# Kernel optimization log

Measured on AMD Instinct MI355X. Metric: run time of the kernel, lower is better.

The kernel has to match this reference:

```python
import jax, jax.numpy as jnp
import numpy as np

N_NODES = 50000
N_EDGES = 1600000
NUM_BASIS = 10
HIDDEN = 64
MAX_RADIUS = 3.0
WEIGHT_NUMEL = 5  # paths: (0x0->0),(0x1->1),(1x0->1),(1x1->0),(1x1->1)


def setup_inputs() -> dict:
    key = jax.random.key(0)
    k1, k2, k3, k4, k5 = jax.random.split(key, 5)
    f_1 = jax.random.normal(k1, (N_NODES, 4), dtype=jnp.float32)
    pos = jax.random.uniform(k2, (N_NODES, 3), dtype=jnp.float32) * MAX_RADIUS
    edge_index = jax.random.randint(k3, (2, N_EDGES), 0, N_NODES, dtype=jnp.int64)
    # radial MLP params (e3nn FullyConnectedNet init: std-normal weights)
    W1 = jax.random.normal(k4, (NUM_BASIS, HIDDEN), dtype=jnp.float32)
    W2 = jax.random.normal(k5, (HIDDEN, WEIGHT_NUMEL), dtype=jnp.float32)
    return {"f_1": f_1, "pos": pos, "W1": W1, "W2": W2, "edge_index": edge_index}


def _forward(f_1, pos, W1, W2, edge_index):
    row, col = edge_index[0], edge_index[1]
    num_nodes = f_1.shape[0]
    num_neighbors = edge_index.shape[1] / num_nodes

    edge_vec = pos[row] - pos[col]                      # [E,3]
    r2 = jnp.sum(edge_vec * edge_vec, axis=-1)
    r = jnp.sqrt(jnp.maximum(r2, 1e-12))                # [E]
    unit = edge_vec / r[:, None]

    # spherical harmonics 0e+1e, component normalization, e3nn (y,z,x) order
    sh = jnp.concatenate(
        [jnp.ones_like(unit[:, :1]), jnp.sqrt(3.0) * unit[:, [1, 2, 0]]], axis=-1
    )                                                   # [E,4]

    # soft_one_hot_linspace, basis='smooth_finite', cutoff=True
    values = jnp.linspace(0.0, MAX_RADIUS, NUM_BASIS + 2)[1:-1]
    step = values[1] - values[0]
    diff = (r[:, None] - values) / step                 # [E,num_basis]
    inside = jnp.abs(diff) < 1.0
    d = jnp.where(inside, diff, 0.0)
    C = 1.14136 * float(np.e) ** 2
    emb = jnp.where(inside, C * jnp.exp(-1.0 / (1.0 + d) - 1.0 / (1.0 - d)), 0.0)

    # e3nn FullyConnectedNet [num_basis, hidden, weight_numel] with relu
    # hidden: act normalized to unit 2nd moment (relu -> *sqrt(2)); weights /sqrt(fan_in)
    h = jax.nn.relu(emb @ (W1 / jnp.sqrt(float(NUM_BASIS)))) * jnp.sqrt(2.0)
    w = h @ (W2 / jnp.sqrt(float(HIDDEN)))              # [E,5]

    # FullyConnectedTensorProduct (0e+1e) x (0e+1e) -> (0e+1e), per-edge weights
    x = f_1[row]
    x0, xv = x[:, 0], x[:, 1:4]
    y0, yv = sh[:, 0], sh[:, 1:4]
    inv_s3 = 1.0 / jnp.sqrt(3.0)
    inv_s6 = 1.0 / jnp.sqrt(6.0)
    # output 0e: fan-in 2 paths -> norm sqrt(1/2)
    out0 = jnp.sqrt(0.5) * (
        w[:, 0] * x0 * y0 + w[:, 3] * jnp.sum(xv * yv, axis=-1) * inv_s3
    )
    # output 1e: fan-in 3 paths -> norm sqrt(3/3)=1
    outv = (
        w[:, 1:2] * x0[:, None] * yv * inv_s3
        + w[:, 2:3] * xv * y0[:, None] * inv_s3
        + w[:, 4:5] * jnp.cross(xv, yv) * inv_s6
    )
    f_edge = jnp.concatenate([out0[:, None], outv], axis=-1)  # [E,4]

    out = jax.ops.segment_sum(f_edge, col, num_segments=num_nodes)
    return out / jnp.sqrt(num_neighbors).astype(out.dtype)


def reference(f_1, pos, W1, W2, edge_index):
    return _forward(f_1, pos, W1, W2, edge_index)
```

## Files before the change

### kernel.cpp

```cpp
#include <hip/hip_runtime.h>
#include <math.h>

#define N_NODES_C 50000
#define N_EDGES_C 1600000
#define EPB3 4096
#define NBLK_E3 391
#define NBLK_N 196
#define TBL 256

#define NREG 49
#define NREGP 64
#define RSH 10
#define RNODES 1024
#define CAPL 16
#define NCHG 16

#define QSCALE 1024.0f
#define QINV   (1.0f / 1024.0f)

__device__ __forceinline__ int detect_is64_block(const void* eidx, int t, int* lds_flag) {
    if (t < 64) {
        const long long* p = (const long long*)eidx;
        bool ok = true;
        for (int k = 0; k < 4; ++k) {
            long long v = p[t * 4 + k];
            ok &= (v >= 0 && v < (long long)N_NODES_C);
        }
        unsigned long long m = __ballot(ok);
        if (t == 0) *lds_flag = (m == ~0ull) ? 1 : 0;
    }
    __syncthreads();
    return *lds_flag;
}

__device__ __forceinline__ int load_col(const void* eidx, int is64, int e) {
    return is64 ? (int)((const long long*)eidx)[N_EDGES_C + e]
                : ((const int*)eidx)[N_EDGES_C + e];
}
__device__ __forceinline__ int load_row(const void* eidx, int is64, int e) {
    return is64 ? (int)((const long long*)eidx)[e]
                : ((const int*)eidx)[e];
}

__device__ __forceinline__ void edge_quant(const float* __restrict__ f1,
                                           const float* __restrict__ pos,
                                           const float* __restrict__ w1s,
                                           const float* __restrict__ W2,
                                           int row, int col, int v[4]) {
    v[0] = v[1] = v[2] = v[3] = 0;
    float px = pos[row * 3 + 0] - pos[col * 3 + 0];
    float py = pos[row * 3 + 1] - pos[col * 3 + 1];
    float pz = pos[row * 3 + 2] - pos[col * 3 + 2];
    float r2 = px * px + py * py + pz * pz;
    float r = sqrtf(fmaxf(r2, 1e-12f));
    float inv_r = 1.0f / r;
    float ux = px * inv_r, uy = py * inv_r, uz = pz * inv_r;
    const float SQ3 = 1.7320508075688772f;
    float yv0 = SQ3 * uy, yv1 = SQ3 * uz, yv2 = SQ3 * ux;

    const float C = 8.433573069075486f;
    float tt = r * (11.0f / 3.0f);
    int k1 = (int)tt;
    float d = tt - (float)k1;
    float e0 = 0.f, e1 = 0.f;
    int b0 = 0, b1 = 0;
    if (k1 >= 1 && k1 <= 10) {
        b0 = k1 - 1;
        e0 = C * __expf(-1.0f / (1.0f + d) - 1.0f / (1.0f - d));
    }
    int k2 = k1 + 1;
    if (k2 <= 10 && d > 0.f) {
        b1 = k2 - 1;
        float d2 = d - 1.0f;
        e1 = C * __expf(-1.0f / (1.0f + d2) - 1.0f / (1.0f - d2));
    }
    if (e0 == 0.f && e1 == 0.f) return;

    const float* r0 = &w1s[b0 * 68];
    const float* r1 = &w1s[b1 * 68];
    float w0 = 0.f, w1a = 0.f, w2a = 0.f, w3 = 0.f, w4 = 0.f;
#pragma unroll
    for (int j = 0; j < 64; j += 4) {
        float4 a = *(const float4*)(r0 + j);
        float4 b = *(const float4*)(r1 + j);
        float h0 = fmaxf(e0 * a.x + e1 * b.x, 0.f);
        float h1 = fmaxf(e0 * a.y + e1 * b.y, 0.f);
        float h2 = fmaxf(e0 * a.z + e1 * b.z, 0.f);
        float h3 = fmaxf(e0 * a.w + e1 * b.w, 0.f);
        w0  += h0 * W2[(j + 0) * 5 + 0] + h1 * W2[(j + 1) * 5 + 0] + h2 * W2[(j + 2) * 5 + 0] + h3 * W2[(j + 3) * 5 + 0];
        w1a += h0 * W2[(j + 0) * 5 + 1] + h1 * W2[(j + 1) * 5 + 1] + h2 * W2[(j + 2) * 5 + 1] + h3 * W2[(j + 3) * 5 + 1];
        w2a += h0 * W2[(j + 0) * 5 + 2] + h1 * W2[(j + 1) * 5 + 2] + h2 * W2[(j + 2) * 5 + 2] + h3 * W2[(j + 3) * 5 + 2];
        w3  += h0 * W2[(j + 0) * 5 + 3] + h1 * W2[(j + 1) * 5 + 3] + h2 * W2[(j + 2) * 5 + 3] + h3 * W2[(j + 3) * 5 + 3];
        w4  += h0 * W2[(j + 0) * 5 + 4] + h1 * W2[(j + 1) * 5 + 4] + h2 * W2[(j + 2) * 5 + 4] + h3 * W2[(j + 3) * 5 + 4];
    }
    const float SC = 0.05590169943749474f;
    w0 *= SC; w1a *= SC; w2a *= SC; w3 *= SC; w4 *= SC;

    float4 x = *(const float4*)(f1 + row * 4);
    float x0 = x.x, xv0 = x.y, xv1 = x.z, xv2 = x.w;

    const float INV_S3 = 0.5773502691896258f;
    const float INV_S6 = 0.4082482904638631f;
    const float SQH    = 0.7071067811865476f;
    const float INV_SQRT_NN = 0.17677669529663687f;

    float dotxy = xv0 * yv0 + xv1 * yv1 + xv2 * yv2;
    float out0 = SQH * (w0 * x0 + w3 * dotxy * INV_S3) * INV_SQRT_NN;
    float cx0 = xv1 * yv2 - xv2 * yv1;
    float cx1 = xv2 * yv0 - xv0 * yv2;
    float cx2 = xv0 * yv1 - xv1 * yv0;
    float o1 = (w1a * x0 * yv0 * INV_S3 + w2a * xv0 * INV_S3 + w4 * cx0 * INV_S6) * INV_SQRT_NN;
    float o2 = (w1a * x0 * yv1 * INV_S3 + w2a * xv1 * INV_S3 + w4 * cx1 * INV_S6) * INV_SQRT_NN;
    float o3 = (w1a * x0 * yv2 * INV_S3 + w2a * xv2 * INV_S3 + w4 * cx2 * INV_S6) * INV_SQRT_NN;

    v[0] = min(8191, max(-8191, (int)rintf(out0 * QSCALE)));
    v[1] = min(8191, max(-8191, (int)rintf(o1   * QSCALE)));
    v[2] = min(8191, max(-8191, (int)rintf(o2   * QSCALE)));
    v[3] = min(8191, max(-8191, (int)rintf(o3   * QSCALE)));
}

__device__ __forceinline__ unsigned long long edge_q(
        float prx, float pry, float prz, float4 xx,
        float pcx, float pcy, float pcz,
        const float* tC0, const float* tC1, const float* tC2,
        const float* tC3, const float* tC4) {
    float px = prx - pcx;
    float py = pry - pcy;
    float pz = prz - pcz;
    float r2 = px * px + py * py + pz * pz;
    float r = sqrtf(fmaxf(r2, 1e-12f));
    float inv_r = 1.0f / r;
    float uv0 = py * inv_r, uv1 = pz * inv_r, uv2 = px * inv_r;

    float ft = fminf(r * (255.0f / 3.0f), 255.0f);
    int idx = min((int)ft, TBL - 2);
    float fr = ft - (float)idx;
    float c0 = fmaf(fr, tC0[idx + 1] - tC0[idx], tC0[idx]);
    float c1 = fmaf(fr, tC1[idx + 1] - tC1[idx], tC1[idx]);
    float c2 = fmaf(fr, tC2[idx + 1] - tC2[idx], tC2[idx]);
    float c3 = fmaf(fr, tC3[idx + 1] - tC3[idx], tC3[idx]);
    float c4 = fmaf(fr, tC4[idx + 1] - tC4[idx], tC4[idx]);

    float x0 = xx.x, xv0 = xx.y, xv1 = xx.z, xv2 = xx.w;

    float dotxy = xv0 * uv0 + xv1 * uv1 + xv2 * uv2;
    float out0 = c0 * x0 + c3 * dotxy;
    float cx0 = xv1 * uv2 - xv2 * uv1;
    float cx1 = xv2 * uv0 - xv0 * uv2;
    float cx2 = xv0 * uv1 - xv1 * uv0;
    float c1x = c1 * x0;
    float o1 = c1x * uv0 + c2 * xv0 + c4 * cx0;
    float o2 = c1x * uv1 + c2 * xv1 + c4 * cx1;
    float o3 = c1x * uv2 + c2 * xv2 + c4 * cx2;

    int v0 = min(8191, max(-8191, (int)rintf(out0 * QSCALE)));
    int v1 = min(8191, max(-8191, (int)rintf(o1 * QSCALE)));
    int v2 = min(8191, max(-8191, (int)rintf(o2 * QSCALE)));
    int v3 = min(8191, max(-8191, (int)rintf(o3 * QSCALE)));

    return (unsigned long long)((long long)v0 + ((long long)v1 << 16)
         + ((long long)v2 << 32) + ((long long)v3 << 48));
}

__global__ __launch_bounds__(1024)
void binscatter_kernel(const float* __restrict__ f1, const float* __restrict__ pos,
                       const float* __restrict__ W1, const float* __restrict__ W2,
                       const void* __restrict__ eidx,
                       unsigned* __restrict__ gOff,
                       unsigned* __restrict__ rcG,
                       float* __restrict__ nodeq,
                       float* __restrict__ tG) {
    __shared__ unsigned rcbuf[EPB3];
    __shared__ unsigned stageRc[EPB3];
    __shared__ unsigned histB[4][NREGP];
    __shared__ unsigned gBaseS[NREGP];
    __shared__ unsigned localBaseS[NREGP];
    __shared__ unsigned cursorLocS[NREGP];
    __shared__ int flag_s;
    const int t = threadIdx.x;
    float* w1s = (float*)stageRc;
    if (blockIdx.x == 0) {
        for (int i = t; i < 640; i += 1024) w1s[(i >> 6) * 68 + (i & 63)] = W1[i];
    }
    if (t < 256) histB[t >> 6][t & 63] = 0u;
    const int is64 = detect_is64_block(eidx, t, &flag_s);

    if (blockIdx.x == 0 && t < TBL) {
        float tt = (float)t * (11.0f / 255.0f);
        int k1 = (int)tt;
        float d = tt - (float)k1;
        const float C = 8.433573069075486f;
        float e0 = 0.f, e1 = 0.f;
        int b0 = 0, b1 = 0;
        if (k1 >= 1 && k1 <= 10) {
            b0 = k1 - 1;
            e0 = C * __expf(-1.0f / (1.0f + d) - 1.0f / (1.0f - d));
        }
        int k2 = k1 + 1;
        if (k2 <= 10 && d > 0.f) {
            b1 = k2 - 1;
            float d2 = d - 1.0f;
            e1 = C * __expf(-1.0f / (1.0f + d2) - 1.0f / (1.0f - d2));
        }
        float w0 = 0.f, w1 = 0.f, w2 = 0.f, w3 = 0.f, w4 = 0.f;
        const float* r0 = &w1s[b0 * 68];
        const float* r1 = &w1s[b1 * 68];
#pragma unroll
        for (int j = 0; j < 64; j += 4) {
            float4 a = *(const float4*)(r0 + j);
            float4 b = *(const float4*)(r1 + j);
            float h0 = fmaxf(e0 * a.x + e1 * b.x, 0.f);
            float h1 = fmaxf(e0 * a.y + e1 * b.y, 0.f);
            float h2 = fmaxf(e0 * a.z + e1 * b.z, 0.f);
            float h3 = fmaxf(e0 * a.w + e1 * b.w, 0.f);
            w0 += h0 * W2[(j + 0) * 5 + 0] + h1 * W2[(j + 1) * 5 + 0] + h2 * W2[(j + 2) * 5 + 0] + h3 * W2[(j + 3) * 5 + 0];
            w1 += h0 * W2[(j + 0) * 5 + 1] + h1 * W2[(j + 1) * 5 + 1] + h2 * W2[(j + 2) * 5 + 1] + h3 * W2[(j + 3) * 5 + 1];
            w2 += h0 * W2[(j + 0) * 5 + 2] + h1 * W2[(j + 1) * 5 + 2] + h2 * W2[(j + 2) * 5 + 2] + h3 * W2[(j + 3) * 5 + 2];
            w3 += h0 * W2[(j + 0) * 5 + 3] + h1 * W2[(j + 1) * 5 + 3] + h2 * W2[(j + 2) * 5 + 3] + h3 * W2[(j + 3) * 5 + 3];
            w4 += h0 * W2[(j + 0) * 5 + 4] + h1 * W2[(j + 1) * 5 + 4] + h2 * W2[(j + 2) * 5 + 4] + h3 * W2[(j + 3) * 5 + 4];
        }
        const float SC  = 0.05590169943749474f;
        const float ISN = 0.17677669529663687f;
        const float SQH = 0.7071067811865476f;
        const float INV_S3 = 0.5773502691896258f;
        const float INV_S6 = 0.4082482904638631f;
        const float SQ3 = 1.7320508075688772f;
        float base = SC * ISN;
        tG[0 * TBL + t] = SQH * base * w0;
        tG[1 * TBL + t] = base * w1;
        tG[2 * TBL + t] = INV_S3 * base * w2;
        tG[3 * TBL + t] = SQH * base * w3;
        tG[4 * TBL + t] = INV_S6 * SQ3 * base * w4;
    }

    const int e0b = blockIdx.x * EPB3;
    const int nedge = min(EPB3, N_EDGES_C - e0b);
    const int hb = (t >> 6) & 3;
    for (int i = t; i < nedge; i += 1024) {
        int row = load_row(eidx, is64, e0b + i);
        int col = load_col(eidx, is64, e0b + i);
        rcbuf[i] = ((unsigned)row << 16) | (unsigned)col;
        atomicAdd(&histB[hb][col >> RSH], 1u);
    }
    {
        int n = blockIdx.x * 1024 + t;
        if (n < N_NODES_C) {
            float4 f = *(const float4*)(f1 + 4 * n);
            float4 p;
            p.x = pos[3 * n + 0];
            p.y = pos[3 * n + 1];
            p.z = pos[3 * n + 2];
            p.w = 0.f;
            *(float4*)(nodeq + 8 * n)     = p;
            *(float4*)(nodeq + 8 * n + 4) = f;
        }
    }
    __syncthreads();
    if (t == 0) {
        unsigned run = 0u;
        for (int b = 0; b < NREGP; ++b) {
            localBaseS[b] = run;
            cursorLocS[b] = run;
            run += histB[0][b] + histB[1][b] + histB[2][b] + histB[3][b];
        }
    }
    if (t < NREGP) {
        unsigned h = histB[0][t] + histB[1][t] + histB[2][t] + histB[3][t];
        gBaseS[t] = ((unsigned)t << CAPL) + atomicAdd(&gOff[t], h);
    }
    __syncthreads();
    for (int i = t; i < nedge; i += 1024) {
        unsigned rc = rcbuf[i];
        int b = (int)((rc & 0xFFFFu) >> RSH);
        unsigned p = atomicAdd(&cursorLocS[b], 1u);
        stageRc[p] = rc;
    }
    __syncthreads();
    for (int i = t; i < nedge; i += 1024) {
        unsigned rc = stageRc[i];
        int b = (int)((rc & 0xFFFFu) >> RSH);
        unsigned dst = gBaseS[b] + ((unsigned)i - localBaseS[b]);
        unsigned lim = ((unsigned)(b + 1)) << CAPL;
        if (dst < lim) rcG[dst] = rc;
    }
}

__global__ __launch_bounds__(256)
void mgather_kernel(const unsigned* __restrict__ rcG,
                    const unsigned* __restrict__ gOff,
                    const float* __restrict__ pos,
                    const float* __restrict__ nodeq,
                    const float* __restrict__ tG,
                    unsigned long long* __restrict__ acc) {
    __shared__ unsigned long long accs[RNODES];
    __shared__ float posx[RNODES];
    __shared__ float posy[RNODES];
    __shared__ float posz[RNODES];
    __shared__ float tC0[TBL];
    __shared__ float tC1[TBL];
    __shared__ float tC2[TBL];
    __shared__ float tC3[TBL];
    __shared__ float tC4[TBL];
    const int t = threadIdx.x;
    const int B = blockIdx.x;
    const int c = blockIdx.y;
    tC0[t] = tG[0 * TBL + t];
    tC1[t] = tG[1 * TBL + t];
    tC2[t] = tG[2 * TBL + t];
    tC3[t] = tG[3 * TBL + t];
    tC4[t] = tG[4 * TBL + t];
    const int nb0 = B << RSH;
    for (int j = t; j < RNODES; j += 256) {
        accs[j] = 0ull;
        int n = nb0 + j;
        if (n < N_NODES_C) {
            posx[j] = pos[3 * n + 0];
            posy[j] = pos[3 * n + 1];
            posz[j] = pos[3 * n + 2];
        }
    }
    __syncthreads();

    unsigned cnt = min(gOff[B], (unsigned)(1u << CAPL));
    unsigned i0 = (unsigned)(((unsigned long long)cnt * (unsigned)c) / NCHG);
    unsigned i1 = (unsigned)(((unsigned long long)cnt * (unsigned)(c + 1)) / NCHG);
    const unsigned* src = rcG + ((size_t)B << CAPL);

    for (unsigned ib = i0 + t; ib < i1; ib += 1024) {
        unsigned ia = ib + 256, ic = ib + 512, id = ib + 768;
        bool va = ia < i1, vb = ic < i1, vc = id < i1;
        unsigned rc0 = src[ib];
        unsigned rc1 = va ? src[ia] : rc0;
        unsigned rc2 = vb ? src[ic] : rc0;
        unsigned rc3 = vc ? src[id] : rc0;
        int row0 = (int)(rc0 >> 16), lc0 = (int)(rc0 & (RNODES - 1));
        int row1 = (int)(rc1 >> 16), lc1 = (int)(rc1 & (RNODES - 1));
        int row2 = (int)(rc2 >> 16), lc2 = (int)(rc2 & (RNODES - 1));
        int row3 = (int)(rc3 >> 16), lc3 = (int)(rc3 & (RNODES - 1));
        const float4* nr0 = (const float4*)(nodeq + ((size_t)row0 << 3));
        const float4* nr1 = (const float4*)(nodeq + ((size_t)row1 << 3));
        const float4* nr2 = (const float4*)(nodeq + ((size_t)row2 << 3));
        const float4* nr3 = (const float4*)(nodeq + ((size_t)row3 << 3));
        float4 pr0 = nr0[0], xx0 = nr0[1];
        float4 pr1 = nr1[0], xx1 = nr1[1];
        float4 pr2 = nr2[0], xx2 = nr2[1];
        float4 pr3 = nr3[0], xx3 = nr3[1];

        unsigned long long Q0 = edge_q(pr0.x, pr0.y, pr0.z, xx0, posx[lc0], posy[lc0], posz[lc0],
                                       tC0, tC1, tC2, tC3, tC4);
        unsigned long long Q1 = edge_q(pr1.x, pr1.y, pr1.z, xx1, posx[lc1], posy[lc1], posz[lc1],
                                       tC0, tC1, tC2, tC3, tC4);
        unsigned long long Q2 = edge_q(pr2.x, pr2.y, pr2.z, xx2, posx[lc2], posy[lc2], posz[lc2],
                                       tC0, tC1, tC2, tC3, tC4);
        unsigned long long Q3 = edge_q(pr3.x, pr3.y, pr3.z, xx3, posx[lc3], posy[lc3], posz[lc3],
                                       tC0, tC1, tC2, tC3, tC4);
        atomicAdd(&accs[lc0], Q0);
        if (va) atomicAdd(&accs[lc1], Q1);
        if (vb) atomicAdd(&accs[lc2], Q2);
        if (vc) atomicAdd(&accs[lc3], Q3);
    }
    __syncthreads();
    for (int j = t; j < RNODES; j += 256) {
        unsigned long long v = accs[j];
        int n = nb0 + j;
        if (v && n < N_NODES_C) {
            __hip_atomic_fetch_add(acc + n, v, __ATOMIC_RELAXED, __HIP_MEMORY_SCOPE_AGENT);
        }
    }
}

__global__ __launch_bounds__(256)
void reduce_unpack(const unsigned long long* __restrict__ acc, float* __restrict__ out) {
    int n = blockIdx.x * 256 + threadIdx.x;
    if (n >= N_NODES_C) return;
    long long T = (long long)acc[n];
    int s0 = (int)(short)(T & 0xFFFF); T = (T - s0) >> 16;
    int s1 = (int)(short)(T & 0xFFFF); T = (T - s1) >> 16;
    int s2 = (int)(short)(T & 0xFFFF); T = (T - s2) >> 16;
    int s3 = (int)T;
    float4 o;
    o.x = (float)s0 * QINV; o.y = (float)s1 * QINV;
    o.z = (float)s2 * QINV; o.w = (float)s3 * QINV;
    *(float4*)(out + 4 * n) = o;
}

__global__ __launch_bounds__(256)
void init_acc(unsigned long long* __restrict__ acc,
              const void* __restrict__ eidx, int* __restrict__ flag) {
    int i = blockIdx.x * 256 + threadIdx.x;
    if (i < N_NODES_C) acc[i] = 0ull;
    if (blockIdx.x == 0 && threadIdx.x < 64) {
        const long long* p = (const long long*)eidx;
        bool ok = true;
        for (int k = 0; k < 4; ++k) {
            long long v = p[threadIdx.x * 4 + k];
            ok &= (v >= 0 && v < (long long)N_NODES_C);
        }
        unsigned long long m = __ballot(ok);
        if (threadIdx.x == 0) *flag = (m == ~0ull) ? 1 : 0;
    }
}

__global__ __launch_bounds__(256)
void equi_conv_atomic(const float* __restrict__ f1, const float* __restrict__ pos,
                      const float* __restrict__ W1, const float* __restrict__ W2,
                      const void* __restrict__ eidx, const int* __restrict__ flag_p,
                      unsigned long long* __restrict__ acc) {
    __shared__ float w1s[10 * 68];
    const int tid = threadIdx.x;
    for (int i = tid; i < 640; i += 256) w1s[(i >> 6) * 68 + (i & 63)] = W1[i];
    __syncthreads();
    const int e = blockIdx.x * 256 + tid;
    if (e >= N_EDGES_C) return;
    const int is64 = *flag_p;
    int row = load_row(eidx, is64, e);
    int col = load_col(eidx, is64, e);
    int v[4];
    edge_quant(f1, pos, w1s, W2, row, col, v);
    if (v[0] | v[1] | v[2] | v[3]) {
        unsigned long long P = (unsigned long long)((long long)v[0] + ((long long)v[1] << 16)
                             + ((long long)v[2] << 32) + ((long long)v[3] << 48));
        __hip_atomic_fetch_add(acc + col, P, __ATOMIC_RELAXED, __HIP_MEMORY_SCOPE_AGENT);
    }
}

extern "C" void kernel_launch(void* const* d_in, const int* in_sizes, int n_in,
                              void* d_out, int out_size, void* d_ws, size_t ws_size,
                              hipStream_t stream) {
    const float* f1  = (const float*)d_in[0];
    const float* pos = (const float*)d_in[1];
    const float* W1  = (const float*)d_in[2];
    const float* W2  = (const float*)d_in[3];
    const void*  eix = d_in[4];
    float* out = (float*)d_out;

    const size_t offRC = 0;
    const size_t szRC  = ((size_t)NREGP << CAPL) * 4;
    const size_t offC  = offRC + szRC;
    const size_t szC   = NREGP * 4;
    const size_t offA  = offC + szC;
    const size_t szA   = (size_t)N_NODES_C * 8;
    const size_t offT  = (offA + szA + 15) & ~(size_t)15;
    const size_t szT   = (size_t)5 * TBL * 4;
    const size_t offQ  = (offT + szT + 15) & ~(size_t)15;
    const size_t szQ   = (size_t)N_NODES_C * 32;
    const size_t need  = offQ + szQ;

    if (ws_size >= need) {
        unsigned*           rcG   = (unsigned*)((char*)d_ws + offRC);
        unsigned*           gOff  = (unsigned*)((char*)d_ws + offC);
        unsigned long long* acc   = (unsigned long long*)((char*)d_ws + offA);
        float*              tG    = (float*)((char*)d_ws + offT);
        float*              nodeq = (float*)((char*)d_ws + offQ);

        hipMemsetAsync(gOff, 0, szC + szA, stream);
        binscatter_kernel<<<NBLK_E3, 1024, 0, stream>>>(f1, pos, W1, W2, eix, gOff, rcG, nodeq, tG);
        mgather_kernel<<<dim3(NREG, NCHG), 256, 0, stream>>>(rcG, gOff, pos, nodeq, tG, acc);
        reduce_unpack<<<NBLK_N, 256, 0, stream>>>(acc, out);
    } else {
        unsigned long long* acc = (unsigned long long*)d_ws;
        int* flag = (int*)((char*)d_ws + (size_t)N_NODES_C * 8);
        const int nblk = (N_NODES_C + 255) / 256;
        init_acc<<<nblk, 256, 0, stream>>>(acc, eix, flag);
        equi_conv_atomic<<<(N_EDGES_C + 255) / 256, 256, 0, stream>>>(f1, pos, W1, W2, eix, flag, acc);
        reduce_unpack<<<nblk, 256, 0, stream>>>(acc, out);
    }
}
```

Before: 104.1 us.

## Replace global bin offsets with fixed per-block cells and fuse final unpack

The scatter kernel now writes each block's edges into a fixed-capacity cell per region and stores per-block counts, so the global atomic offset counters go away. The accumulator zeroing moves into the scatter kernel, which removes the memset. The final unpack is folded into the gather kernel through a last-block-done counter per region, which removes the third launch. The gather loop now walks cells one wave at a time without the 4-way unrolling, which may lower memory-level parallelism. A cell holding more than its fixed capacity of 168 edges silently drops the extra edges.

After: 160.9 us. 1.55x slower.

```diff
diff --git a/kernel.cpp b/kernel.cpp
--- a/kernel.cpp
+++ b/kernel.cpp
@@ -5,14 +5,13 @@
 #define N_EDGES_C 1600000
 #define EPB3 4096
 #define NBLK_E3 391
-#define NBLK_N 196
 #define TBL 256
 
 #define NREG 49
 #define NREGP 64
 #define RSH 10
 #define RNODES 1024
-#define CAPL 16
+#define CAP 168
 #define NCHG 16
 
 #define QSCALE 1024.0f
@@ -166,14 +165,15 @@
 void binscatter_kernel(const float* __restrict__ f1, const float* __restrict__ pos,
                        const float* __restrict__ W1, const float* __restrict__ W2,
                        const void* __restrict__ eidx,
-                       unsigned* __restrict__ gOff,
                        unsigned* __restrict__ rcG,
+                       unsigned short* __restrict__ countsG,
                        float* __restrict__ nodeq,
-                       float* __restrict__ tG) {
+                       float* __restrict__ tG,
+                       unsigned long long* __restrict__ acc,
+                       unsigned* __restrict__ doneB) {
     __shared__ unsigned rcbuf[EPB3];
     __shared__ unsigned stageRc[EPB3];
     __shared__ unsigned histB[4][NREGP];
-    __shared__ unsigned gBaseS[NREGP];
     __shared__ unsigned localBaseS[NREGP];
     __shared__ unsigned cursorLocS[NREGP];
     __shared__ int flag_s;
@@ -183,6 +183,11 @@
         for (int i = t; i < 640; i += 1024) w1s[(i >> 6) * 68 + (i & 63)] = W1[i];
     }
     if (t < 256) histB[t >> 6][t & 63] = 0u;
+    if (t < 128) {
+        int n = blockIdx.x * 128 + t;
+        if (n < N_NODES_C) acc[n] = 0ull;
+    }
+    if (blockIdx.x == 0 && t >= 128 && t < 192) doneB[t - 128] = 0u;
     const int is64 = detect_is64_block(eidx, t, &flag_s);
 
     if (blockIdx.x == 0 && t < TBL) {
@@ -266,7 +271,7 @@
     }
     if (t < NREGP) {
         unsigned h = histB[0][t] + histB[1][t] + histB[2][t] + histB[3][t];
-        gBaseS[t] = ((unsigned)t << CAPL) + atomicAdd(&gOff[t], h);
+        countsG[blockIdx.x * NREGP + t] = (unsigned short)min(h, (unsigned)CAP);
     }
     __syncthreads();
     for (int i = t; i < nedge; i += 1024) {
@@ -279,19 +284,22 @@
     for (int i = t; i < nedge; i += 1024) {
         unsigned rc = stageRc[i];
         int b = (int)((rc & 0xFFFFu) >> RSH);
-        unsigned dst = gBaseS[b] + ((unsigned)i - localBaseS[b]);
-        unsigned lim = ((unsigned)(b + 1)) << CAPL;
-        if (dst < lim) rcG[dst] = rc;
+        unsigned idx = (unsigned)i - localBaseS[b];
+        if (idx < CAP) {
+            rcG[((size_t)b * NBLK_E3 + blockIdx.x) * CAP + idx] = rc;
+        }
     }
 }
 
 __global__ __launch_bounds__(256)
 void mgather_kernel(const unsigned* __restrict__ rcG,
-                    const unsigned* __restrict__ gOff,
+                    const unsigned short* __restrict__ countsG,
                     const float* __restrict__ pos,
                     const float* __restrict__ nodeq,
                     const float* __restrict__ tG,
-                    unsigned long long* __restrict__ acc) {
+                    unsigned long long* __restrict__ acc,
+                    unsigned* __restrict__ doneB,
+                    float* __restrict__ out) {
     __shared__ unsigned long long accs[RNODES];
     __shared__ float posx[RNODES];
     __shared__ float posy[RNODES];
@@ -301,6 +309,7 @@
     __shared__ float tC2[TBL];
     __shared__ float tC3[TBL];
     __shared__ float tC4[TBL];
+    __shared__ int last_s;
     const int t = threadIdx.x;
     const int B = blockIdx.x;
     const int c = blockIdx.y;
@@ -321,43 +330,23 @@
     }
     __syncthreads();
 
-    unsigned cnt = min(gOff[B], (unsigned)(1u << CAPL));
-    unsigned i0 = (unsigned)(((unsigned long long)cnt * (unsigned)c) / NCHG);
-    unsigned i1 = (unsigned)(((unsigned long long)cnt * (unsigned)(c + 1)) / NCHG);
-    const unsigned* src = rcG + ((size_t)B << CAPL);
-
-    for (unsigned ib = i0 + t; ib < i1; ib += 1024) {
-        unsigned ia = ib + 256, ic = ib + 512, id = ib + 768;
-        bool va = ia < i1, vb = ic < i1, vc = id < i1;
-        unsigned rc0 = src[ib];
-        unsigned rc1 = va ? src[ia] : rc0;
-        unsigned rc2 = vb ? src[ic] : rc0;
-        unsigned rc3 = vc ? src[id] : rc0;
-        int row0 = (int)(rc0 >> 16), lc0 = (int)(rc0 & (RNODES - 1));
-        int row1 = (int)(rc1 >> 16), lc1 = (int)(rc1 & (RNODES - 1));
-        int row2 = (int)(rc2 >> 16), lc2 = (int)(rc2 & (RNODES - 1));
-        int row3 = (int)(rc3 >> 16), lc3 = (int)(rc3 & (RNODES - 1));
-        const float4* nr0 = (const float4*)(nodeq + ((size_t)row0 << 3));
-        const float4* nr1 = (const float4*)(nodeq + ((size_t)row1 << 3));
-        const float4* nr2 = (const float4*)(nodeq + ((size_t)row2 << 3));
-        const float4* nr3 = (const float4*)(nodeq + ((size_t)row3 << 3));
-        float4 pr0 = nr0[0], xx0 = nr0[1];
-        float4 pr1 = nr1[0], xx1 = nr1[1];
-        float4 pr2 = nr2[0], xx2 = nr2[1];
-        float4 pr3 = nr3[0], xx3 = nr3[1];
-
-        unsigned long long Q0 = edge_q(pr0.x, pr0.y, pr0.z, xx0, posx[lc0], posy[lc0], posz[lc0],
-                                       tC0, tC1, tC2, tC3, tC4);
-        unsigned long long Q1 = edge_q(pr1.x, pr1.y, pr1.z, xx1, posx[lc1], posy[lc1], posz[lc1],
-                                       tC0, tC1, tC2, tC3, tC4);
-        unsigned long long Q2 = edge_q(pr2.x, pr2.y, pr2.z, xx2, posx[lc2], posy[lc2], posz[lc2],
-                                       tC0, tC1, tC2, tC3, tC4);
-        unsigned long long Q3 = edge_q(pr3.x, pr3.y, pr3.z, xx3, posx[lc3], posy[lc3], posz[lc3],
-                                       tC0, tC1, tC2, tC3, tC4);
-        atomicAdd(&accs[lc0], Q0);
-        if (va) atomicAdd(&accs[lc1], Q1);
-        if (vb) atomicAdd(&accs[lc2], Q2);
-        if (vc) atomicAdd(&accs[lc3], Q3);
+    const int k0 = (c * NBLK_E3) / NCHG;
+    const int k1 = ((c + 1) * NBLK_E3) / NCHG;
+    const int wave = t >> 6, lane = t & 63;
+    for (int k = k0 + wave; k < k1; k += 4) {
+        unsigned cnt = countsG[k * NREGP + B];
+        const unsigned* cell = rcG + ((size_t)B * NBLK_E3 + k) * CAP;
+        for (unsigned i = lane; i < cnt; i += 64) {
+            unsigned rc = cell[i];
+            int row = (int)(rc >> 16), lc = (int)(rc & (RNODES - 1));
+            const float4* nr = (const float4*)(nodeq + ((size_t)row << 3));
+            float4 pr = nr[0];
+            float4 xx = nr[1];
+            unsigned long long Q = edge_q(pr.x, pr.y, pr.z, xx,
+                                          posx[lc], posy[lc], posz[lc],
+                                          tC0, tC1, tC2, tC3, tC4);
+            atomicAdd(&accs[lc], Q);
+        }
     }
     __syncthreads();
     for (int j = t; j < RNODES; j += 256) {
@@ -366,6 +355,48 @@
         if (v && n < N_NODES_C) {
             __hip_atomic_fetch_add(acc + n, v, __ATOMIC_RELAXED, __HIP_MEMORY_SCOPE_AGENT);
         }
+    }
+    __threadfence();
+    if (t == 0) {
+        unsigned old = __hip_atomic_fetch_add(doneB + B, 1u, __ATOMIC_ACQ_REL,
+                                              __HIP_MEMORY_SCOPE_AGENT);
+        last_s = (old == (unsigned)(NCHG - 1));
+    }
+    __syncthreads();
+    if (last_s) {
+        __threadfence();
+        for (int j = t; j < RNODES; j += 256) {
+            int n = nb0 + j;
+            if (n >= N_NODES_C) continue;
+            unsigned long long s = __hip_atomic_load(acc + n, __ATOMIC_RELAXED,
+                                                     __HIP_MEMORY_SCOPE_AGENT);
+            long long T = (long long)s;
+            int s0 = (int)(short)(T & 0xFFFF); T = (T - s0) >> 16;
+            int s1 = (int)(short)(T & 0xFFFF); T = (T - s1) >> 16;
+            int s2 = (int)(short)(T & 0xFFFF); T = (T - s2) >> 16;
+            int s3 = (int)T;
+            float4 o;
+            o.x = (float)s0 * QINV; o.y = (float)s1 * QINV;
+            o.z = (float)s2 * QINV; o.w = (float)s3 * QINV;
+            *(float4*)(out + 4 * n) = o;
+        }
+    }
+}
+
+__global__ __launch_bounds__(256)
+void init_acc(unsigned long long* __restrict__ acc,
+              const void* __restrict__ eidx, int* __restrict__ flag) {
+    int i = blockIdx.x * 256 + threadIdx.x;
+    if (i < N_NODES_C) acc[i] = 0ull;
+    if (blockIdx.x == 0 && threadIdx.x < 64) {
+        const long long* p = (const long long*)eidx;
+        bool ok = true;
+        for (int k = 0; k < 4; ++k) {
+            long long v = p[threadIdx.x * 4 + k];
+            ok &= (v >= 0 && v < (long long)N_NODES_C);
+        }
+        unsigned long long m = __ballot(ok);
+        if (threadIdx.x == 0) *flag = (m == ~0ull) ? 1 : 0;
     }
 }
 
@@ -385,23 +416,6 @@
 }
 
 __global__ __launch_bounds__(256)
-void init_acc(unsigned long long* __restrict__ acc,
-              const void* __restrict__ eidx, int* __restrict__ flag) {
-    int i = blockIdx.x * 256 + threadIdx.x;
-    if (i < N_NODES_C) acc[i] = 0ull;
-    if (blockIdx.x == 0 && threadIdx.x < 64) {
-        const long long* p = (const long long*)eidx;
-        bool ok = true;
-        for (int k = 0; k < 4; ++k) {
-            long long v = p[threadIdx.x * 4 + k];
-            ok &= (v >= 0 && v < (long long)N_NODES_C);
-        }
-        unsigned long long m = __ballot(ok);
-        if (threadIdx.x == 0) *flag = (m == ~0ull) ? 1 : 0;
-    }
-}
-
-__global__ __launch_bounds__(256)
 void equi_conv_atomic(const float* __restrict__ f1, const float* __restrict__ pos,
                       const float* __restrict__ W1, const float* __restrict__ W2,
                       const void* __restrict__ eidx, const int* __restrict__ flag_p,
@@ -435,28 +449,31 @@
     float* out = (float*)d_out;
 
     const size_t offRC = 0;
-    const size_t szRC  = ((size_t)NREGP << CAPL) * 4;
-    const size_t offC  = offRC + szRC;
-    const size_t szC   = NREGP * 4;
-    const size_t offA  = offC + szC;
+    const size_t szRC  = (size_t)NREG * NBLK_E3 * CAP * 4;
+    const size_t offK  = (offRC + szRC + 15) & ~(size_t)15;
+    const size_t szK   = (size_t)NBLK_E3 * NREGP * 2;
+    const size_t offA  = (offK + szK + 15) & ~(size_t)15;
     const size_t szA   = (size_t)N_NODES_C * 8;
-    const size_t offT  = (offA + szA + 15) & ~(size_t)15;
+    const size_t offD  = (offA + szA + 15) & ~(size_t)15;
+    const size_t szD   = 64 * 4;
+    const size_t offT  = (offD + szD + 15) & ~(size_t)15;
     const size_t szT   = (size_t)5 * TBL * 4;
     const size_t offQ  = (offT + szT + 15) & ~(size_t)15;
     const size_t szQ   = (size_t)N_NODES_C * 32;
     const size_t need  = offQ + szQ;
 
     if (ws_size >= need) {
-        unsigned*           rcG   = (unsigned*)((char*)d_ws + offRC);
-        unsigned*           gOff  = (unsigned*)((char*)d_ws + offC);
-        unsigned long long* acc   = (unsigned long long*)((char*)d_ws + offA);
-        float*              tG    = (float*)((char*)d_ws + offT);
-        float*              nodeq = (float*)((char*)d_ws + offQ);
-
-        hipMemsetAsync(gOff, 0, szC + szA, stream);
-        binscatter_kernel<<<NBLK_E3, 1024, 0, stream>>>(f1, pos, W1, W2, eix, gOff, rcG, nodeq, tG);
-        mgather_kernel<<<dim3(NREG, NCHG), 256, 0, stream>>>(rcG, gOff, pos, nodeq, tG, acc);
-        reduce_unpack<<<NBLK_N, 256, 0, stream>>>(acc, out);
+        unsigned*           rcG     = (unsigned*)((char*)d_ws + offRC);
+        unsigned short*     countsG = (unsigned short*)((char*)d_ws + offK);
+        unsigned long long* acc     = (unsigned long long*)((char*)d_ws + offA);
+        unsigned*           doneB   = (unsigned*)((char*)d_ws + offD);
+        float*              tG      = (float*)((char*)d_ws + offT);
+        float*              nodeq   = (float*)((char*)d_ws + offQ);
+
+        binscatter_kernel<<<NBLK_E3, 1024, 0, stream>>>(f1, pos, W1, W2, eix,
+                                                        rcG, countsG, nodeq, tG, acc, doneB);
+        mgather_kernel<<<dim3(NREG, NCHG), 256, 0, stream>>>(rcG, countsG, pos, nodeq, tG,
+                                                             acc, doneB, out);
     } else {
         unsigned long long* acc = (unsigned long long*)d_ws;
         int* flag = (int*)((char*)d_ws + (size_t)N_NODES_C * 8);
```
